# Kernel tuning notes

Hardware: AMD Instinct MI355X
Metric: run time of the kernel (lower is better)

The kernel has to match this reference:

```python
import jax, jax.numpy as jnp
import numpy as np

N = 50000      # total nodes (250 graphs x 200 nodes, per forward_nodes_batched default)
E = 800000     # directed edges, avg degree 16
IN = 128       # in_dim
H = 128        # hidden
G = 250        # number of graphs


def setup_inputs() -> dict:
    key = jax.random.key(0)
    k_x, k_e, k_w1, k_w2 = jax.random.split(key, 4)
    x = jax.random.normal(k_x, (N, IN), dtype=jnp.float32)
    edge_index = jax.random.randint(k_e, (2, E), 0, N, dtype=jnp.int32)
    batch = jnp.repeat(jnp.arange(G, dtype=jnp.int32), N // G)  # 200 nodes per graph
    # GCNConv params (glorot-style scale)
    W1 = jax.random.normal(k_w1, (IN, H), dtype=jnp.float32) * (1.0 / np.sqrt(IN))
    b1 = jnp.zeros((H,), dtype=jnp.float32)
    W2 = jax.random.normal(k_w2, (H, H), dtype=jnp.float32) * (1.0 / np.sqrt(H))
    b2 = jnp.zeros((H,), dtype=jnp.float32)
    return {"x": x, "W1": W1, "b1": b1, "W2": W2, "b2": b2,
            "edge_index": edge_index, "batch": batch}


def _gcn_conv(x, W, b, src, dst, norm, n):
    # PyG GCNConv: x' = W x, then scatter-add of norm * x'_src into dst, + bias
    h = x @ W                                   # [n, H]
    msg = h[src] * norm[:, None]                # [E', H] gather + scale
    agg = jax.ops.segment_sum(msg, dst, num_segments=n)
    return agg + b


def reference(x, W1, b1, W2, b2, edge_index, batch):
    n = x.shape[0]
    # add self-loops (PyG GCNConv default add_self_loops=True)
    loops = jnp.arange(n, dtype=edge_index.dtype)
    src = jnp.concatenate([edge_index[0], loops])
    dst = jnp.concatenate([edge_index[1], loops])
    # symmetric normalization deg^-1/2[src] * deg^-1/2[dst], deg on target index
    deg = jax.ops.segment_sum(jnp.ones_like(dst, dtype=x.dtype), dst, num_segments=n)
    dinv = jnp.where(deg > 0, jax.lax.rsqrt(deg), 0.0)
    norm = dinv[src] * dinv[dst]
    # two conv layers, ELU activation; dropout is identity in eval mode
    h = jax.nn.elu(_gcn_conv(x, W1, b1, src, dst, norm, n))
    h = jax.nn.elu(_gcn_conv(h, W2, b2, src, dst, norm, n))
    # global mean pool over batch segment ids
    ones = jnp.ones((n,), dtype=x.dtype)
    cnt = jax.ops.segment_sum(ones, batch, num_segments=G)
    s = jax.ops.segment_sum(h, batch, num_segments=G)
    return s / jnp.clip(cnt, 1.0)[:, None]
```

## Files before the change

### kernel.cpp

```cpp
#include <hip/hip_runtime.h>
#include <hip/hip_fp16.h>
#include <math.h>

#define FDIM 128
#define MAXDEG 64

typedef _Float16 f16x8 __attribute__((ext_vector_type(8)));
typedef float f32x4 __attribute__((ext_vector_type(4)));

static inline size_t align512(size_t x) { return (x + 511) & ~((size_t)511); }

__global__ __launch_bounds__(256) void prep_kernel(int* __restrict__ cnt, int n,
                                                   const float* __restrict__ W1,
                                                   const float* __restrict__ W2,
                                                   __half* __restrict__ W1t,
                                                   __half* __restrict__ W2t, int zb) {
    int b = blockIdx.x;
    if (b < zb) {
        int i = b * 256 + threadIdx.x;
        if (i < n) cnt[i] = 0;
        return;
    }
    int q = b - zb;
    const float* W = (q < 64) ? W1 : W2;
    __half* Wt = (q < 64) ? W1t : W2t;
    int gid = (q & 63) * 256 + threadIdx.x;
    int c = gid >> 7, k = gid & 127;
    Wt[(size_t)c * FDIM + k] = __float2half(W[(size_t)k * FDIM + c]);
}

__global__ __launch_bounds__(256) void gemm_edges(const float* __restrict__ X,
                                                  const __half* __restrict__ Wt,
                                                  __half* __restrict__ out, int nrows,
                                                  int gemm_blocks,
                                                  const int* __restrict__ src,
                                                  const int* __restrict__ dstE,
                                                  int* __restrict__ cnt,
                                                  int* __restrict__ bucket, int ne) {
    __shared__ __half Xl[64 * 136];
    if ((int)blockIdx.x >= gemm_blocks) {
        int base = (((int)blockIdx.x - gemm_blocks) * 256 + threadIdx.x) * 4;
        if (base + 3 < ne) {
            int4 s4 = *(const int4*)(src + base);
            int4 d4 = *(const int4*)(dstE + base);
            int k0 = atomicAdd(&cnt[d4.x], 1);
            int k1 = atomicAdd(&cnt[d4.y], 1);
            int k2 = atomicAdd(&cnt[d4.z], 1);
            int k3 = atomicAdd(&cnt[d4.w], 1);
            if (k0 < MAXDEG) bucket[(size_t)d4.x * MAXDEG + k0] = s4.x;
            if (k1 < MAXDEG) bucket[(size_t)d4.y * MAXDEG + k1] = s4.y;
            if (k2 < MAXDEG) bucket[(size_t)d4.z * MAXDEG + k2] = s4.z;
            if (k3 < MAXDEG) bucket[(size_t)d4.w * MAXDEG + k3] = s4.w;
        } else {
            for (int i = base; i < ne; i++) {
                int d = dstE[i], s = src[i];
                int k = atomicAdd(&cnt[d], 1);
                if (k < MAXDEG) bucket[(size_t)d * MAXDEG + k] = s;
            }
        }
        return;
    }
    int tid = threadIdx.x;
    int row0 = blockIdx.x * 64;

    for (int i = tid; i < 64 * 32; i += 256) {
        int r = i >> 5, c4 = i & 31;
        int rg = row0 + r;
        if (rg > nrows - 1) rg = nrows - 1;
        float4 v = *(const float4*)(X + (size_t)rg * FDIM + c4 * 4);
        union { __half2 h[2]; int2 i2; } u;
        u.h[0] = __floats2half2_rn(v.x, v.y);
        u.h[1] = __floats2half2_rn(v.z, v.w);
        *(int2*)(&Xl[r * 136 + c4 * 4]) = u.i2;
    }
    __syncthreads();

    int lane = tid & 63;
    int w = tid >> 6;
    int l15 = lane & 15;
    int kq = lane >> 4;

    f16x8 a[4];
    #pragma unroll
    for (int kk = 0; kk < 4; kk++)
        a[kk] = *(const f16x8*)(&Xl[(w * 16 + l15) * 136 + kk * 32 + kq * 8]);
    __syncthreads();

    #pragma unroll
    for (int c = 0; c < 8; c++) {
        f32x4 acc = {0.f, 0.f, 0.f, 0.f};
        #pragma unroll
        for (int kk = 0; kk < 4; kk++) {
            f16x8 b = *(const f16x8*)(Wt + (size_t)(c * 16 + l15) * FDIM + kk * 32 + kq * 8);
            acc = __builtin_amdgcn_mfma_f32_16x16x32_f16(a[kk], b, acc, 0, 0, 0);
        }
        #pragma unroll
        for (int r = 0; r < 4; r++)
            Xl[(w * 16 + kq * 4 + r) * 136 + c * 16 + l15] = __float2half(acc[r]);
    }
    __syncthreads();

    #pragma unroll
    for (int it = 0; it < 2; it++) {
        int i = it * 256 + tid;
        int r = i >> 3, seg = i & 7;
        int rowg = row0 + r;
        if (rowg < nrows) {
            int4 v0 = *(const int4*)(&Xl[r * 136 + seg * 16]);
            int4 v1 = *(const int4*)(&Xl[r * 136 + seg * 16 + 8]);
            int4* p = (int4*)(out + (size_t)rowg * FDIM + seg * 16);
            p[0] = v0; p[1] = v1;
        }
    }
}

__global__ void dinv_kernel(const int* __restrict__ cnt, float* __restrict__ dinv, int n) {
    int i = blockIdx.x * 256 + threadIdx.x;
    if (i < n) dinv[i] = 1.0f / sqrtf((float)(cnt[i] + 1));
}

#define ACC_EDGE(S, R)                                                   \
{                                                                        \
    float d = dinv[S];                                                   \
    __half2 h; float2 f;                                                 \
    h = *(__half2*)&R.x; f = __half22float2(h);                          \
    acc[0] = fmaf(d, f.x, acc[0]); acc[1] = fmaf(d, f.y, acc[1]);        \
    h = *(__half2*)&R.y; f = __half22float2(h);                          \
    acc[2] = fmaf(d, f.x, acc[2]); acc[3] = fmaf(d, f.y, acc[3]);        \
    h = *(__half2*)&R.z; f = __half22float2(h);                          \
    acc[4] = fmaf(d, f.x, acc[4]); acc[5] = fmaf(d, f.y, acc[5]);        \
    h = *(__half2*)&R.w; f = __half22float2(h);                          \
    acc[6] = fmaf(d, f.x, acc[6]); acc[7] = fmaf(d, f.y, acc[7]);        \
}

__global__ __launch_bounds__(256) void agg_gemm(const __half* __restrict__ G,
                                                const int* __restrict__ bucket,
                                                const int* __restrict__ cnt,
                                                const float* __restrict__ dinv,
                                                const float* __restrict__ bias,
                                                const __half* __restrict__ Wt,
                                                __half* __restrict__ out, int nrows) {
    __shared__ __half Xl[32 * 136];
    int tid = threadIdx.x;
    int row0 = blockIdx.x * 32;
    const float4* G4 = (const float4*)G;

    int c = tid & 15;
    const float4* b4 = (const float4*)bias;
    float4 blo = b4[2 * c], bhi = b4[2 * c + 1];

    for (int g = 0; g < 2; g++) {
        int r = g * 16 + (tid >> 4);
        int node = row0 + r;
        if (node > nrows - 1) node = nrows - 1;
        int deg = cnt[node]; if (deg > MAXDEG) deg = MAXDEG;
        const int* bk = bucket + (size_t)node * MAXDEG;
        float dn = dinv[node];

        float acc[8];
        {
            float4 sraw = G4[(size_t)node * 16 + c];
            __half2 h; float2 f;
            h = *(__half2*)&sraw.x; f = __half22float2(h); acc[0] = dn * f.x; acc[1] = dn * f.y;
            h = *(__half2*)&sraw.y; f = __half22float2(h); acc[2] = dn * f.x; acc[3] = dn * f.y;
            h = *(__half2*)&sraw.z; f = __half22float2(h); acc[4] = dn * f.x; acc[5] = dn * f.y;
            h = *(__half2*)&sraw.w; f = __half22float2(h); acc[6] = dn * f.x; acc[7] = dn * f.y;
        }
        int e = 0;
        for (; e + 3 < deg; e += 4) {
            int s0 = bk[e], s1 = bk[e + 1], s2 = bk[e + 2], s3 = bk[e + 3];
            float4 r0 = G4[(size_t)s0 * 16 + c];
            float4 r1 = G4[(size_t)s1 * 16 + c];
            float4 r2 = G4[(size_t)s2 * 16 + c];
            float4 r3 = G4[(size_t)s3 * 16 + c];
            ACC_EDGE(s0, r0) ACC_EDGE(s1, r1) ACC_EDGE(s2, r2) ACC_EDGE(s3, r3)
        }
        for (; e < deg; e++) {
            int s = bk[e];
            float4 rr = G4[(size_t)s * 16 + c];
            ACC_EDGE(s, rr)
        }
        float v[8];
        v[0] = fmaf(dn, acc[0], blo.x); v[1] = fmaf(dn, acc[1], blo.y);
        v[2] = fmaf(dn, acc[2], blo.z); v[3] = fmaf(dn, acc[3], blo.w);
        v[4] = fmaf(dn, acc[4], bhi.x); v[5] = fmaf(dn, acc[5], bhi.y);
        v[6] = fmaf(dn, acc[6], bhi.z); v[7] = fmaf(dn, acc[7], bhi.w);
        #pragma unroll
        for (int j = 0; j < 8; j++) v[j] = (v[j] > 0.f) ? v[j] : expm1f(v[j]);
        union { __half2 h[4]; int4 i4; } u;
        u.h[0] = __floats2half2_rn(v[0], v[1]);
        u.h[1] = __floats2half2_rn(v[2], v[3]);
        u.h[2] = __floats2half2_rn(v[4], v[5]);
        u.h[3] = __floats2half2_rn(v[6], v[7]);
        *(int4*)(&Xl[r * 136 + c * 8]) = u.i4;
    }
    __syncthreads();

    int lane = tid & 63;
    int w = tid >> 6;
    int l15 = lane & 15;
    int kq = lane >> 4;
    int rb = (w & 1) * 16;
    int ctb = (w >> 1) * 4;

    f16x8 a[4];
    #pragma unroll
    for (int kk = 0; kk < 4; kk++)
        a[kk] = *(const f16x8*)(&Xl[(rb + l15) * 136 + kk * 32 + kq * 8]);
    __syncthreads();

    #pragma unroll
    for (int cc = 0; cc < 4; cc++) {
        int ct = ctb + cc;
        f32x4 acc2 = {0.f, 0.f, 0.f, 0.f};
        #pragma unroll
        for (int kk = 0; kk < 4; kk++) {
            f16x8 b = *(const f16x8*)(Wt + (size_t)(ct * 16 + l15) * FDIM + kk * 32 + kq * 8);
            acc2 = __builtin_amdgcn_mfma_f32_16x16x32_f16(a[kk], b, acc2, 0, 0, 0);
        }
        #pragma unroll
        for (int r = 0; r < 4; r++)
            Xl[(rb + kq * 4 + r) * 136 + ct * 16 + l15] = __float2half(acc2[r]);
    }
    __syncthreads();

    {
        int i = tid;
        int r = i >> 3, seg = i & 7;
        int rowg = row0 + r;
        if (rowg < nrows) {
            int4 v0 = *(const int4*)(&Xl[r * 136 + seg * 16]);
            int4 v1 = *(const int4*)(&Xl[r * 136 + seg * 16 + 8]);
            int4* p = (int4*)(out + (size_t)rowg * FDIM + seg * 16);
            p[0] = v0; p[1] = v1;
        }
    }
}

__global__ __launch_bounds__(256) void agg_elu(const __half* __restrict__ G,
                                               const int* __restrict__ bucket,
                                               const int* __restrict__ cnt,
                                               const float* __restrict__ dinv,
                                               const float* __restrict__ bias,
                                               float* __restrict__ out, int n) {
    int node = blockIdx.x * 16 + (threadIdx.x >> 4);
    int c = threadIdx.x & 15;
    if (node >= n) return;
    const float4* G4 = (const float4*)G;
    int deg = cnt[node]; if (deg > MAXDEG) deg = MAXDEG;
    const int* bk = bucket + (size_t)node * MAXDEG;
    float dn = dinv[node];

    float acc[8];
    {
        float4 sraw = G4[(size_t)node * 16 + c];
        __half2 h; float2 f;
        h = *(__half2*)&sraw.x; f = __half22float2(h); acc[0] = dn * f.x; acc[1] = dn * f.y;
        h = *(__half2*)&sraw.y; f = __half22float2(h); acc[2] = dn * f.x; acc[3] = dn * f.y;
        h = *(__half2*)&sraw.z; f = __half22float2(h); acc[4] = dn * f.x; acc[5] = dn * f.y;
        h = *(__half2*)&sraw.w; f = __half22float2(h); acc[6] = dn * f.x; acc[7] = dn * f.y;
    }
    int e = 0;
    for (; e + 3 < deg; e += 4) {
        int s0 = bk[e], s1 = bk[e + 1], s2 = bk[e + 2], s3 = bk[e + 3];
        float4 r0 = G4[(size_t)s0 * 16 + c];
        float4 r1 = G4[(size_t)s1 * 16 + c];
        float4 r2 = G4[(size_t)s2 * 16 + c];
        float4 r3 = G4[(size_t)s3 * 16 + c];
        ACC_EDGE(s0, r0) ACC_EDGE(s1, r1) ACC_EDGE(s2, r2) ACC_EDGE(s3, r3)
    }
    for (; e < deg; e++) {
        int s = bk[e];
        float4 rr = G4[(size_t)s * 16 + c];
        ACC_EDGE(s, rr)
    }

    const float4* b4 = (const float4*)bias;
    float4 blo = b4[2 * c], bhi = b4[2 * c + 1];
    float4 vlo, vhi;
    vlo.x = fmaf(dn, acc[0], blo.x); vlo.y = fmaf(dn, acc[1], blo.y);
    vlo.z = fmaf(dn, acc[2], blo.z); vlo.w = fmaf(dn, acc[3], blo.w);
    vhi.x = fmaf(dn, acc[4], bhi.x); vhi.y = fmaf(dn, acc[5], bhi.y);
    vhi.z = fmaf(dn, acc[6], bhi.z); vhi.w = fmaf(dn, acc[7], bhi.w);
    vlo.x = (vlo.x > 0.f) ? vlo.x : expm1f(vlo.x);
    vlo.y = (vlo.y > 0.f) ? vlo.y : expm1f(vlo.y);
    vlo.z = (vlo.z > 0.f) ? vlo.z : expm1f(vlo.z);
    vlo.w = (vlo.w > 0.f) ? vlo.w : expm1f(vlo.w);
    vhi.x = (vhi.x > 0.f) ? vhi.x : expm1f(vhi.x);
    vhi.y = (vhi.y > 0.f) ? vhi.y : expm1f(vhi.y);
    vhi.z = (vhi.z > 0.f) ? vhi.z : expm1f(vhi.z);
    vhi.w = (vhi.w > 0.f) ? vhi.w : expm1f(vhi.w);
    float4* o4 = (float4*)out;
    o4[(size_t)node * 32 + 2 * c] = vlo;
    o4[(size_t)node * 32 + 2 * c + 1] = vhi;
}

__global__ __launch_bounds__(256) void pool_kernel(const float* __restrict__ H,
                                                   float* __restrict__ out,
                                                   int nper, int ngraphs) {
    __shared__ float tmp[128];
    int g = blockIdx.x;
    int f = threadIdx.x & 127;
    int half = threadIdx.x >> 7;
    if (g >= ngraphs) return;
    const float* base = H + (size_t)g * nper * FDIM;
    float acc = 0.f;
    for (int i = half; i < nper; i += 2) acc += base[(size_t)i * FDIM + f];
    if (half == 1) tmp[f] = acc;
    __syncthreads();
    if (half == 0) out[(size_t)g * FDIM + f] = (acc + tmp[f]) * (1.0f / (float)nper);
}

extern "C" void kernel_launch(void* const* d_in, const int* in_sizes, int n_in,
                              void* d_out, int out_size, void* d_ws, size_t ws_size,
                              hipStream_t stream) {
    const float* x  = (const float*)d_in[0];
    const float* W1 = (const float*)d_in[1];
    const float* b1 = (const float*)d_in[2];
    const float* W2 = (const float*)d_in[3];
    const float* b2 = (const float*)d_in[4];
    const int* edge_index = (const int*)d_in[5];
    float* out = (float*)d_out;

    int N = in_sizes[0] / FDIM;
    int E = in_sizes[5] / 2;
    int G = out_size / FDIM;
    int nper = N / G;
    const int* src = edge_index;
    const int* dst = edge_index + E;

    char* ws = (char*)d_ws;
    size_t off = 0;
    int* cnt = (int*)(ws + off);        off = align512(off + (size_t)N * 4);
    float* dinv = (float*)(ws + off);   off = align512(off + (size_t)N * 4);
    __half* W1t = (__half*)(ws + off);  off = align512(off + (size_t)FDIM * FDIM * 2);
    __half* W2t = (__half*)(ws + off);  off = align512(off + (size_t)FDIM * FDIM * 2);
    int* bucket = (int*)(ws + off);     off = align512(off + (size_t)N * MAXDEG * 4);
    __half* bufG = (__half*)(ws + off); off = align512(off + (size_t)N * FDIM * 2);
    __half* bufH = (__half*)(ws + off); off = align512(off + (size_t)N * FDIM * 2);
    float* bufB = (float*)(ws + off);   off = align512(off + (size_t)N * FDIM * 4);
    (void)ws_size;

    int nb = (N + 255) / 256;
    int gemm_grid = (N + 63) / 64;
    int ag_grid = (N + 31) / 32;
    int agg_grid = (N + 15) / 16;
    int e4_grid = (E / 4 + 255) / 256;

    prep_kernel<<<nb + 128, 256, 0, stream>>>(cnt, N, W1, W2, W1t, W2t, nb);
    gemm_edges<<<gemm_grid + e4_grid, 256, 0, stream>>>(
        x, W1t, bufG, N, gemm_grid, src, dst, cnt, bucket, E);
    dinv_kernel<<<nb, 256, 0, stream>>>(cnt, dinv, N);
    agg_gemm<<<ag_grid, 256, 0, stream>>>(bufG, bucket, cnt, dinv, b1, W2t, bufH, N);
    agg_elu<<<agg_grid, 256, 0, stream>>>(bufH, bucket, cnt, dinv, b2, bufB, N);
    pool_kernel<<<G, 256, 0, stream>>>(bufB, out, nper, G);
}
```

Before: 166.3 us.

## Pre-scale features by source dinv, vectorize index loads, store layer-2 output in fp16

Moves the per-edge source normalization out of the gather loops. The layer-1 features are pre-multiplied by dinv in a new scale_dinv kernel, and the agg_gemm GEMM epilogue multiplies its output by the row's dinv. This removes the per-edge dinv gather, and the neighbor loop now loads indices with int4 and unrolls 8 edges. The final activations are written as fp16 and pooled from fp16, which halves that traffic at some precision cost. The extra rescale pass rereads and rewrites bufG.

New measurement: 164.4 us. Within noise of the previous version (-1.1%).

```diff
diff --git a/kernel.cpp b/kernel.cpp
--- a/kernel.cpp
+++ b/kernel.cpp
@@ -114,23 +114,26 @@
     }
 }
 
-__global__ void dinv_kernel(const int* __restrict__ cnt, float* __restrict__ dinv, int n) {
-    int i = blockIdx.x * 256 + threadIdx.x;
-    if (i < n) dinv[i] = 1.0f / sqrtf((float)(cnt[i] + 1));
-}
-
-#define ACC_EDGE(S, R)                                                   \
+__global__ __launch_bounds__(256) void scale_dinv(const int* __restrict__ cnt,
+                                                  float* __restrict__ dinv,
+                                                  __half* __restrict__ G, int n) {
+    int row = blockIdx.x * 4 + (threadIdx.x >> 6);
+    int c = threadIdx.x & 63;
+    if (row >= n) return;
+    float dv = 1.0f / sqrtf((float)(cnt[row] + 1));
+    if (c == 0) dinv[row] = dv;
+    __half2* p = (__half2*)(G + (size_t)row * FDIM) + c;
+    float2 f = __half22float2(*p);
+    *p = __floats2half2_rn(f.x * dv, f.y * dv);
+}
+
+#define ACC_ROW(R)                                                       \
 {                                                                        \
-    float d = dinv[S];                                                   \
     __half2 h; float2 f;                                                 \
-    h = *(__half2*)&R.x; f = __half22float2(h);                          \
-    acc[0] = fmaf(d, f.x, acc[0]); acc[1] = fmaf(d, f.y, acc[1]);        \
-    h = *(__half2*)&R.y; f = __half22float2(h);                          \
-    acc[2] = fmaf(d, f.x, acc[2]); acc[3] = fmaf(d, f.y, acc[3]);        \
-    h = *(__half2*)&R.z; f = __half22float2(h);                          \
-    acc[4] = fmaf(d, f.x, acc[4]); acc[5] = fmaf(d, f.y, acc[5]);        \
-    h = *(__half2*)&R.w; f = __half22float2(h);                          \
-    acc[6] = fmaf(d, f.x, acc[6]); acc[7] = fmaf(d, f.y, acc[7]);        \
+    h = *(__half2*)&R.x; f = __half22float2(h); acc[0] += f.x; acc[1] += f.y; \
+    h = *(__half2*)&R.y; f = __half22float2(h); acc[2] += f.x; acc[3] += f.y; \
+    h = *(__half2*)&R.z; f = __half22float2(h); acc[4] += f.x; acc[5] += f.y; \
+    h = *(__half2*)&R.w; f = __half22float2(h); acc[6] += f.x; acc[7] += f.y; \
 }
 
 __global__ __launch_bounds__(256) void agg_gemm(const __half* __restrict__ G,
@@ -161,24 +164,30 @@
         {
             float4 sraw = G4[(size_t)node * 16 + c];
             __half2 h; float2 f;
-            h = *(__half2*)&sraw.x; f = __half22float2(h); acc[0] = dn * f.x; acc[1] = dn * f.y;
-            h = *(__half2*)&sraw.y; f = __half22float2(h); acc[2] = dn * f.x; acc[3] = dn * f.y;
-            h = *(__half2*)&sraw.z; f = __half22float2(h); acc[4] = dn * f.x; acc[5] = dn * f.y;
-            h = *(__half2*)&sraw.w; f = __half22float2(h); acc[6] = dn * f.x; acc[7] = dn * f.y;
+            h = *(__half2*)&sraw.x; f = __half22float2(h); acc[0] = f.x; acc[1] = f.y;
+            h = *(__half2*)&sraw.y; f = __half22float2(h); acc[2] = f.x; acc[3] = f.y;
+            h = *(__half2*)&sraw.z; f = __half22float2(h); acc[4] = f.x; acc[5] = f.y;
+            h = *(__half2*)&sraw.w; f = __half22float2(h); acc[6] = f.x; acc[7] = f.y;
         }
         int e = 0;
-        for (; e + 3 < deg; e += 4) {
-            int s0 = bk[e], s1 = bk[e + 1], s2 = bk[e + 2], s3 = bk[e + 3];
-            float4 r0 = G4[(size_t)s0 * 16 + c];
-            float4 r1 = G4[(size_t)s1 * 16 + c];
-            float4 r2 = G4[(size_t)s2 * 16 + c];
-            float4 r3 = G4[(size_t)s3 * 16 + c];
-            ACC_EDGE(s0, r0) ACC_EDGE(s1, r1) ACC_EDGE(s2, r2) ACC_EDGE(s3, r3)
+        for (; e + 7 < deg; e += 8) {
+            int4 i0 = *(const int4*)(bk + e);
+            int4 i1 = *(const int4*)(bk + e + 4);
+            float4 r0 = G4[(size_t)i0.x * 16 + c];
+            float4 r1 = G4[(size_t)i0.y * 16 + c];
+            float4 r2 = G4[(size_t)i0.z * 16 + c];
+            float4 r3 = G4[(size_t)i0.w * 16 + c];
+            float4 r4 = G4[(size_t)i1.x * 16 + c];
+            float4 r5 = G4[(size_t)i1.y * 16 + c];
+            float4 r6 = G4[(size_t)i1.z * 16 + c];
+            float4 r7 = G4[(size_t)i1.w * 16 + c];
+            ACC_ROW(r0) ACC_ROW(r1) ACC_ROW(r2) ACC_ROW(r3)
+            ACC_ROW(r4) ACC_ROW(r5) ACC_ROW(r6) ACC_ROW(r7)
         }
         for (; e < deg; e++) {
             int s = bk[e];
             float4 rr = G4[(size_t)s * 16 + c];
-            ACC_EDGE(s, rr)
+            ACC_ROW(rr)
         }
         float v[8];
         v[0] = fmaf(dn, acc[0], blo.x); v[1] = fmaf(dn, acc[1], blo.y);
@@ -209,6 +218,13 @@
         a[kk] = *(const f16x8*)(&Xl[(rb + l15) * 136 + kk * 32 + kq * 8]);
     __syncthreads();
 
+    float dsc[4];
+    #pragma unroll
+    for (int r = 0; r < 4; r++) {
+        int rowg = row0 + rb + kq * 4 + r;
+        dsc[r] = dinv[(rowg < nrows) ? rowg : (nrows - 1)];
+    }
+
     #pragma unroll
     for (int cc = 0; cc < 4; cc++) {
         int ct = ctb + cc;
@@ -220,7 +236,7 @@
         }
         #pragma unroll
         for (int r = 0; r < 4; r++)
-            Xl[(rb + kq * 4 + r) * 136 + ct * 16 + l15] = __float2half(acc2[r]);
+            Xl[(rb + kq * 4 + r) * 136 + ct * 16 + l15] = __float2half(acc2[r] * dsc[r]);
     }
     __syncthreads();
 
@@ -242,7 +258,7 @@
                                                const int* __restrict__ cnt,
                                                const float* __restrict__ dinv,
                                                const float* __restrict__ bias,
-                                               float* __restrict__ out, int n) {
+                                               __half* __restrict__ out, int n) {
     int node = blockIdx.x * 16 + (threadIdx.x >> 4);
     int c = threadIdx.x & 15;
     if (node >= n) return;
@@ -255,60 +271,71 @@
     {
         float4 sraw = G4[(size_t)node * 16 + c];
         __half2 h; float2 f;
-        h = *(__half2*)&sraw.x; f = __half22float2(h); acc[0] = dn * f.x; acc[1] = dn * f.y;
-        h = *(__half2*)&sraw.y; f = __half22float2(h); acc[2] = dn * f.x; acc[3] = dn * f.y;
-        h = *(__half2*)&sraw.z; f = __half22float2(h); acc[4] = dn * f.x; acc[5] = dn * f.y;
-        h = *(__half2*)&sraw.w; f = __half22float2(h); acc[6] = dn * f.x; acc[7] = dn * f.y;
+        h = *(__half2*)&sraw.x; f = __half22float2(h); acc[0] = f.x; acc[1] = f.y;
+        h = *(__half2*)&sraw.y; f = __half22float2(h); acc[2] = f.x; acc[3] = f.y;
+        h = *(__half2*)&sraw.z; f = __half22float2(h); acc[4] = f.x; acc[5] = f.y;
+        h = *(__half2*)&sraw.w; f = __half22float2(h); acc[6] = f.x; acc[7] = f.y;
     }
     int e = 0;
-    for (; e + 3 < deg; e += 4) {
-        int s0 = bk[e], s1 = bk[e + 1], s2 = bk[e + 2], s3 = bk[e + 3];
-        float4 r0 = G4[(size_t)s0 * 16 + c];
-        float4 r1 = G4[(size_t)s1 * 16 + c];
-        float4 r2 = G4[(size_t)s2 * 16 + c];
-        float4 r3 = G4[(size_t)s3 * 16 + c];
-        ACC_EDGE(s0, r0) ACC_EDGE(s1, r1) ACC_EDGE(s2, r2) ACC_EDGE(s3, r3)
+    for (; e + 7 < deg; e += 8) {
+        int4 i0 = *(const int4*)(bk + e);
+        int4 i1 = *(const int4*)(bk + e + 4);
+        float4 r0 = G4[(size_t)i0.x * 16 + c];
+        float4 r1 = G4[(size_t)i0.y * 16 + c];
+        float4 r2 = G4[(size_t)i0.z * 16 + c];
+        float4 r3 = G4[(size_t)i0.w * 16 + c];
+        float4 r4 = G4[(size_t)i1.x * 16 + c];
+        float4 r5 = G4[(size_t)i1.y * 16 + c];
+        float4 r6 = G4[(size_t)i1.z * 16 + c];
+        float4 r7 = G4[(size_t)i1.w * 16 + c];
+        ACC_ROW(r0) ACC_ROW(r1) ACC_ROW(r2) ACC_ROW(r3)
+        ACC_ROW(r4) ACC_ROW(r5) ACC_ROW(r6) ACC_ROW(r7)
     }
     for (; e < deg; e++) {
         int s = bk[e];
         float4 rr = G4[(size_t)s * 16 + c];
-        ACC_EDGE(s, rr)
+        ACC_ROW(rr)
     }
 
     const float4* b4 = (const float4*)bias;
     float4 blo = b4[2 * c], bhi = b4[2 * c + 1];
-    float4 vlo, vhi;
-    vlo.x = fmaf(dn, acc[0], blo.x); vlo.y = fmaf(dn, acc[1], blo.y);
-    vlo.z = fmaf(dn, acc[2], blo.z); vlo.w = fmaf(dn, acc[3], blo.w);
-    vhi.x = fmaf(dn, acc[4], bhi.x); vhi.y = fmaf(dn, acc[5], bhi.y);
-    vhi.z = fmaf(dn, acc[6], bhi.z); vhi.w = fmaf(dn, acc[7], bhi.w);
-    vlo.x = (vlo.x > 0.f) ? vlo.x : expm1f(vlo.x);
-    vlo.y = (vlo.y > 0.f) ? vlo.y : expm1f(vlo.y);
-    vlo.z = (vlo.z > 0.f) ? vlo.z : expm1f(vlo.z);
-    vlo.w = (vlo.w > 0.f) ? vlo.w : expm1f(vlo.w);
-    vhi.x = (vhi.x > 0.f) ? vhi.x : expm1f(vhi.x);
-    vhi.y = (vhi.y > 0.f) ? vhi.y : expm1f(vhi.y);
-    vhi.z = (vhi.z > 0.f) ? vhi.z : expm1f(vhi.z);
-    vhi.w = (vhi.w > 0.f) ? vhi.w : expm1f(vhi.w);
-    float4* o4 = (float4*)out;
-    o4[(size_t)node * 32 + 2 * c] = vlo;
-    o4[(size_t)node * 32 + 2 * c + 1] = vhi;
-}
-
-__global__ __launch_bounds__(256) void pool_kernel(const float* __restrict__ H,
+    float v[8];
+    v[0] = fmaf(dn, acc[0], blo.x); v[1] = fmaf(dn, acc[1], blo.y);
+    v[2] = fmaf(dn, acc[2], blo.z); v[3] = fmaf(dn, acc[3], blo.w);
+    v[4] = fmaf(dn, acc[4], bhi.x); v[5] = fmaf(dn, acc[5], bhi.y);
+    v[6] = fmaf(dn, acc[6], bhi.z); v[7] = fmaf(dn, acc[7], bhi.w);
+    #pragma unroll
+    for (int j = 0; j < 8; j++) v[j] = (v[j] > 0.f) ? v[j] : expm1f(v[j]);
+    union { __half2 h[4]; int4 i4; } u;
+    u.h[0] = __floats2half2_rn(v[0], v[1]);
+    u.h[1] = __floats2half2_rn(v[2], v[3]);
+    u.h[2] = __floats2half2_rn(v[4], v[5]);
+    u.h[3] = __floats2half2_rn(v[6], v[7]);
+    ((int4*)(out + (size_t)node * FDIM))[c] = u.i4;
+}
+
+__global__ __launch_bounds__(256) void pool_kernel(const __half* __restrict__ H,
                                                    float* __restrict__ out,
                                                    int nper, int ngraphs) {
-    __shared__ float tmp[128];
+    __shared__ float2 tmp[4][64];
     int g = blockIdx.x;
-    int f = threadIdx.x & 127;
-    int half = threadIdx.x >> 7;
+    int cp = threadIdx.x & 63;
+    int q = threadIdx.x >> 6;
     if (g >= ngraphs) return;
-    const float* base = H + (size_t)g * nper * FDIM;
-    float acc = 0.f;
-    for (int i = half; i < nper; i += 2) acc += base[(size_t)i * FDIM + f];
-    if (half == 1) tmp[f] = acc;
-    __syncthreads();
-    if (half == 0) out[(size_t)g * FDIM + f] = (acc + tmp[f]) * (1.0f / (float)nper);
+    const __half2* base = (const __half2*)(H + (size_t)g * nper * FDIM) + cp;
+    float2 acc = make_float2(0.f, 0.f);
+    for (int i = q; i < nper; i += 4) {
+        float2 f = __half22float2(base[(size_t)i * 64]);
+        acc.x += f.x; acc.y += f.y;
+    }
+    tmp[q][cp] = acc;
+    __syncthreads();
+    if (q == 0) {
+        float2 a = tmp[0][cp], b = tmp[1][cp], c2 = tmp[2][cp], d = tmp[3][cp];
+        float inv = 1.0f / (float)nper;
+        out[(size_t)g * FDIM + cp * 2]     = (a.x + b.x + c2.x + d.x) * inv;
+        out[(size_t)g * FDIM + cp * 2 + 1] = (a.y + b.y + c2.y + d.y) * inv;
+    }
 }
 
 extern "C" void kernel_launch(void* const* d_in, const int* in_sizes, int n_in,
@@ -331,14 +358,14 @@
 
     char* ws = (char*)d_ws;
     size_t off = 0;
-    int* cnt = (int*)(ws + off);        off = align512(off + (size_t)N * 4);
-    float* dinv = (float*)(ws + off);   off = align512(off + (size_t)N * 4);
-    __half* W1t = (__half*)(ws + off);  off = align512(off + (size_t)FDIM * FDIM * 2);
-    __half* W2t = (__half*)(ws + off);  off = align512(off + (size_t)FDIM * FDIM * 2);
-    int* bucket = (int*)(ws + off);     off = align512(off + (size_t)N * MAXDEG * 4);
-    __half* bufG = (__half*)(ws + off); off = align512(off + (size_t)N * FDIM * 2);
-    __half* bufH = (__half*)(ws + off); off = align512(off + (size_t)N * FDIM * 2);
-    float* bufB = (float*)(ws + off);   off = align512(off + (size_t)N * FDIM * 4);
+    int* cnt = (int*)(ws + off);         off = align512(off + (size_t)N * 4);
+    float* dinv = (float*)(ws + off);    off = align512(off + (size_t)N * 4);
+    __half* W1t = (__half*)(ws + off);   off = align512(off + (size_t)FDIM * FDIM * 2);
+    __half* W2t = (__half*)(ws + off);   off = align512(off + (size_t)FDIM * FDIM * 2);
+    int* bucket = (int*)(ws + off);      off = align512(off + (size_t)N * MAXDEG * 4);
+    __half* bufG = (__half*)(ws + off);  off = align512(off + (size_t)N * FDIM * 2);
+    __half* bufH = (__half*)(ws + off);  off = align512(off + (size_t)N * FDIM * 2);
+    __half* bufBh = (__half*)(ws + off); off = align512(off + (size_t)N * FDIM * 2);
     (void)ws_size;
 
     int nb = (N + 255) / 256;
@@ -350,8 +377,8 @@
     prep_kernel<<<nb + 128, 256, 0, stream>>>(cnt, N, W1, W2, W1t, W2t, nb);
     gemm_edges<<<gemm_grid + e4_grid, 256, 0, stream>>>(
         x, W1t, bufG, N, gemm_grid, src, dst, cnt, bucket, E);
-    dinv_kernel<<<nb, 256, 0, stream>>>(cnt, dinv, N);
+    scale_dinv<<<(N + 3) / 4, 256, 0, stream>>>(cnt, dinv, bufG, N);
     agg_gemm<<<ag_grid, 256, 0, stream>>>(bufG, bucket, cnt, dinv, b1, W2t, bufH, N);
-    agg_elu<<<agg_grid, 256, 0, stream>>>(bufH, bucket, cnt, dinv, b2, bufB, N);
-    pool_kernel<<<G, 256, 0, stream>>>(bufB, out, nper, G);
-}
+    agg_elu<<<agg_grid, 256, 0, stream>>>(bufH, bucket, cnt, dinv, b2, bufBh, N);
+    pool_kernel<<<G, 256, 0, stream>>>(bufBh, out, nper, G);
+}
```
